# Kernel tuning notes

Measured on AMD Instinct MI355X. Metric: run time of the kernel, lower is better.

Reference implementation:

```python
import jax, jax.numpy as jnp
import numpy as np

N_NODES = 100000
N_EDGES = 1600000
D_IN = 64
D_HID = 64
D_OUT = 64
DROP_P = 0.5


def _degree_norms(src, dst, n):
    ones = jnp.ones(src.shape[0], dtype=jnp.float32)
    deg_out = jax.ops.segment_sum(ones, src, num_segments=n)  # out-degree of src nodes
    deg_in = jax.ops.segment_sum(ones, dst, num_segments=n)   # in-degree of dst nodes
    norm_src = jnp.where(deg_out > 0, jax.lax.rsqrt(jnp.maximum(deg_out, 1.0)), 0.0)
    norm_dst = jnp.where(deg_in > 0, jax.lax.rsqrt(jnp.maximum(deg_in, 1.0)), 0.0)
    return norm_src, norm_dst


def _graph_conv(h, W, b, src, dst, norm_src, norm_dst, n, activation=None):
    # DGL GraphConv, norm='both': out = D_in^{-1/2} A (D_out^{-1/2} h) W + b
    h = h * norm_src[:, None]
    h = h @ W                      # small GEMM first (in >= out), math-equivalent
    msg = h[src]                   # gather  [E, d]
    agg = jax.ops.segment_sum(msg, dst, num_segments=n)  # scatter-add [N, d]
    out = agg * norm_dst[:, None] + b
    if activation is not None:
        out = activation(out)
    return out


def _dropout(h, key, p=DROP_P):
    keep = jax.random.bernoulli(key, 1.0 - p, h.shape)
    return jnp.where(keep, h / (1.0 - p), 0.0)


def setup_inputs() -> dict:
    key = jax.random.key(0)
    ks = jax.random.split(key, 6)
    x = jax.random.normal(ks[0], (N_NODES, D_IN), dtype=jnp.float32)
    W0 = jax.random.normal(ks[1], (D_IN, D_HID), dtype=jnp.float32) * 0.05
    W1 = jax.random.normal(ks[2], (D_HID, D_HID), dtype=jnp.float32) * 0.05
    W2 = jax.random.normal(ks[3], (D_HID, D_OUT), dtype=jnp.float32) * 0.05
    b0 = jnp.zeros((D_HID,), dtype=jnp.float32)
    b1 = jnp.zeros((D_HID,), dtype=jnp.float32)
    b2 = jnp.zeros((D_OUT,), dtype=jnp.float32)
    src = jax.random.randint(ks[4], (N_EDGES,), 0, N_NODES, dtype=jnp.int32)
    dst = jax.random.randint(ks[5], (N_EDGES,), 0, N_NODES, dtype=jnp.int32)
    return {"x": x, "W0": W0, "b0": b0, "W1": W1, "b1": b1, "W2": W2, "b2": b2,
            "src": src, "dst": dst}


def reference(x, W0, b0, W1, b1, W2, b2, src, dst):
    n = x.shape[0]
    norm_src, norm_dst = _degree_norms(src, dst, n)
    dk = jax.random.key(1)
    h = _graph_conv(x, W0, b0, src, dst, norm_src, norm_dst, n, jax.nn.relu)
    h = _dropout(h, jax.random.fold_in(dk, 0))
    h = _graph_conv(h, W1, b1, src, dst, norm_src, norm_dst, n, jax.nn.relu)
    h = _dropout(h, jax.random.fold_in(dk, 1))
    h = _graph_conv(h, W2, b2, src, dst, norm_src, norm_dst, n, None)
    return h
```

## Files before the change

### kernel.cpp

```cpp
#include <hip/hip_runtime.h>
#include <hip/hip_bf16.h>
#include <hip/hip_fp16.h>
#include <cstddef>


#define WG 256
#define SLOT_S 48
#define NB_SHIFT 9
#define NB_W 512
#define EB 2048
#define PSTRIDE 257

__host__ __device__ static inline unsigned rotl32(unsigned x, int r) {
  return (x << r) | (x >> (32 - r));
}

__host__ __device__ static inline void threefry2x32(unsigned k0, unsigned k1,
                                                    unsigned x0, unsigned x1,
                                                    unsigned& o0, unsigned& o1) {
  unsigned ks2 = k0 ^ k1 ^ 0x1BD11BDAu;
  x0 += k0; x1 += k1;
#define TF_ROUND(r) { x0 += x1; x1 = rotl32(x1, r); x1 ^= x0; }
  TF_ROUND(13) TF_ROUND(15) TF_ROUND(26) TF_ROUND(6)
  x0 += k1;  x1 += ks2 + 1u;
  TF_ROUND(17) TF_ROUND(29) TF_ROUND(16) TF_ROUND(24)
  x0 += ks2; x1 += k0 + 2u;
  TF_ROUND(13) TF_ROUND(15) TF_ROUND(26) TF_ROUND(6)
  x0 += k0;  x1 += k1 + 3u;
  TF_ROUND(17) TF_ROUND(29) TF_ROUND(16) TF_ROUND(24)
  x0 += k1;  x1 += ks2 + 4u;
  TF_ROUND(13) TF_ROUND(15) TF_ROUND(26) TF_ROUND(6)
  x0 += ks2; x1 += k0 + 5u;
#undef TF_ROUND
  o0 = x0; o1 = x1;
}

__device__ static inline float2 h2f(unsigned u) {
  return __half22float2(__builtin_bit_cast(__half2, u));
}
__device__ static inline unsigned f2h(float a, float b) {
  return __builtin_bit_cast(unsigned, __floats2half2_rn(a, b));
}


__global__ __launch_bounds__(WG) void bin_k(
    const int* __restrict__ src, const int* __restrict__ dst,
    unsigned* __restrict__ binbuf_d, unsigned short* __restrict__ binbuf_s,
    unsigned short* __restrict__ pref_d, unsigned short* __restrict__ pref_s,
    int e) {
  __shared__ int hist_d[256], hist_s[256];
  __shared__ int scan_d[256], scan_s[256];
  __shared__ int curs_d[256], curs_s[256];
  __shared__ unsigned sorted_d[EB];
  __shared__ unsigned short sorted_s[EB];
  int tid = threadIdx.x;
  int blk = blockIdx.x;
  int base = blk * EB;
  int cnt = e - base;
  if (cnt > EB) cnt = EB;

  hist_d[tid] = 0;
  hist_s[tid] = 0;
  __syncthreads();
  for (int i = tid; i < cnt; i += WG) {
    int d = dst[base + i];
    int s = src[base + i];
    atomicAdd(&hist_d[d >> NB_SHIFT], 1);
    atomicAdd(&hist_s[s >> NB_SHIFT], 1);
  }
  __syncthreads();
  int hd = hist_d[tid], hs = hist_s[tid];
  scan_d[tid] = hd;
  scan_s[tid] = hs;
  __syncthreads();
  for (int st = 1; st < 256; st <<= 1) {
    int ad = (tid >= st) ? scan_d[tid - st] : 0;
    int as = (tid >= st) ? scan_s[tid - st] : 0;
    __syncthreads();
    scan_d[tid] += ad;
    scan_s[tid] += as;
    __syncthreads();
  }
  int ed = scan_d[tid] - hd;
  int es = scan_s[tid] - hs;
  curs_d[tid] = ed;
  curs_s[tid] = es;
  pref_d[(size_t)blk * PSTRIDE + tid] = (unsigned short)ed;
  pref_s[(size_t)blk * PSTRIDE + tid] = (unsigned short)es;
  if (tid == 255) {
    pref_d[(size_t)blk * PSTRIDE + 256] = (unsigned short)scan_d[255];
    pref_s[(size_t)blk * PSTRIDE + 256] = (unsigned short)scan_s[255];
  }
  __syncthreads();
  for (int i = tid; i < cnt; i += WG) {
    int d = dst[base + i];
    int s = src[base + i];
    int pd = atomicAdd(&curs_d[d >> NB_SHIFT], 1);
    sorted_d[pd] = ((unsigned)(d & (NB_W - 1)) << 17) | (unsigned)s;
    int ps = atomicAdd(&curs_s[s >> NB_SHIFT], 1);
    sorted_s[ps] = (unsigned short)(s & (NB_W - 1));
  }
  __syncthreads();
  for (int i = tid; i < cnt; i += WG) binbuf_d[base + i] = sorted_d[i];
  for (int i = tid; i < cnt; i += WG) binbuf_s[base + i] = sorted_s[i];
}


__global__ __launch_bounds__(WG) void debin_k(
    const unsigned* __restrict__ binbuf_d,
    const unsigned short* __restrict__ binbuf_s,
    const unsigned short* __restrict__ pref_d,
    const unsigned short* __restrict__ pref_s,
    int* __restrict__ slot, int* __restrict__ cnt_in,
    float* __restrict__ nsrc, const float* __restrict__ x,
    unsigned short* __restrict__ G0, int n, int nblk, int nbuck) {
  __shared__ int lcnt[NB_W];
  __shared__ float lns[NB_W];
  int tid = threadIdx.x;
  int b = blockIdx.x;
  for (int i = tid; i < NB_W; i += WG) lcnt[i] = 0;
  __syncthreads();
  if (b < nbuck) {
    for (int seg = tid; seg < nblk; seg += WG) {
      const unsigned short* pr = pref_d + (size_t)seg * PSTRIDE + b;
      int p0 = pr[0], p1 = pr[1];
      const unsigned* bb = binbuf_d + (size_t)seg * EB;
      for (int i = p0; i < p1; ++i) {
        unsigned v = bb[i];
        int dl = v >> 17;
        int s = (int)(v & 0x1FFFFu);
        int c = atomicAdd(&lcnt[dl], 1);
        if (c < SLOT_S) slot[(size_t)((b << NB_SHIFT) + dl) * SLOT_S + c] = s;
      }
    }
    __syncthreads();
    for (int i = tid; i < NB_W; i += WG) {
      int v = (b << NB_SHIFT) + i;
      if (v < n) cnt_in[v] = lcnt[i];
    }
  } else {
    int b2 = b - nbuck;
    for (int seg = tid; seg < nblk; seg += WG) {
      const unsigned short* pr = pref_s + (size_t)seg * PSTRIDE + b2;
      int p0 = pr[0], p1 = pr[1];
      const unsigned short* bb = binbuf_s + (size_t)seg * EB;
      for (int i = p0; i < p1; ++i) atomicAdd(&lcnt[bb[i]], 1);
    }
    __syncthreads();
    int vbase = b2 << NB_SHIFT;
    for (int i = tid; i < NB_W; i += WG) {
      int v = vbase + i;
      if (v < n) {
        int c = lcnt[i];
        float ns = (c > 0) ? rsqrtf((float)c) : 0.f;
        lns[i] = ns;
        nsrc[v] = ns;
      }
    }
    __syncthreads();
    const float4* x4 = (const float4*)x;
    uint2* G2 = (uint2*)G0;
    int lim = NB_W * 16;
    for (int idx = tid; idx < lim; idx += WG) {
      int nl = idx >> 4;
      int v = vbase + nl;
      if (v < n) {
        float ns = lns[nl];
        float4 r = x4[(size_t)v * 16 + (idx & 15)];
        G2[(size_t)v * 16 + (idx & 15)] =
            make_uint2(f2h(r.x * ns, r.y * ns), f2h(r.z * ns, r.w * ns));
      }
    }
  }
}

__global__ __launch_bounds__(WG) void layer_k(
    const unsigned short* __restrict__ G, const int* __restrict__ slot,
    const int* __restrict__ cnt_in, const float* __restrict__ nsrc,
    const float* __restrict__ W, const float* __restrict__ bias,
    unsigned short* __restrict__ GoutH, float* __restrict__ GoutF,
    int n, int mid, unsigned dk0, unsigned dk1) {
  __shared__ float4 Ws[1024];
  __shared__ __align__(16) float rows[4][272];
  const float4* W4 = (const float4*)W;
  for (int i = threadIdx.x; i < 1024; i += WG) Ws[i] = W4[i];

  int wave = threadIdx.x >> 6;
  int lane = threadIdx.x & 63;
  int g = lane >> 4;
  int l16 = lane & 15;
  int v = blockIdx.x * 16 + wave * 4 + g;
  bool valid = (v < n);
  int vc = valid ? v : (n - 1);

  int degt = valid ? cnt_in[vc] : 0;
  int deg = (degt > SLOT_S) ? SLOT_S : degt;
  const int* sl = slot + (size_t)vc * SLOT_S;
  const uint2* G2 = (const uint2*)G;

  float4 aA = make_float4(0.f, 0.f, 0.f, 0.f);
  float4 aB = make_float4(0.f, 0.f, 0.f, 0.f);
  float4 aC = make_float4(0.f, 0.f, 0.f, 0.f);
  float4 aD = make_float4(0.f, 0.f, 0.f, 0.f);
#define ACC(dst, m) { float2 lo = h2f((m).x), hi = h2f((m).y); \
    dst.x += lo.x; dst.y += lo.y; dst.z += hi.x; dst.w += hi.y; }
  int nq = deg >> 2;
  int i = 0;
  for (; i + 1 < nq; i += 2) {
    int4 q0 = *(const int4*)(sl + i * 4);
    int4 q1 = *(const int4*)(sl + i * 4 + 4);
    uint2 m0 = G2[(size_t)q0.x * 16 + l16];
    uint2 m1 = G2[(size_t)q0.y * 16 + l16];
    uint2 m2 = G2[(size_t)q0.z * 16 + l16];
    uint2 m3 = G2[(size_t)q0.w * 16 + l16];
    uint2 m4 = G2[(size_t)q1.x * 16 + l16];
    uint2 m5 = G2[(size_t)q1.y * 16 + l16];
    uint2 m6 = G2[(size_t)q1.z * 16 + l16];
    uint2 m7 = G2[(size_t)q1.w * 16 + l16];
    ACC(aA, m0) ACC(aB, m1) ACC(aC, m2) ACC(aD, m3)
    ACC(aA, m4) ACC(aB, m5) ACC(aC, m6) ACC(aD, m7)
  }
  if (i < nq) {
    int4 q0 = *(const int4*)(sl + i * 4);
    uint2 m0 = G2[(size_t)q0.x * 16 + l16];
    uint2 m1 = G2[(size_t)q0.y * 16 + l16];
    uint2 m2 = G2[(size_t)q0.z * 16 + l16];
    uint2 m3 = G2[(size_t)q0.w * 16 + l16];
    ACC(aA, m0) ACC(aB, m1) ACC(aC, m2) ACC(aD, m3)
  }
  int rem = deg & 3;
  if (rem) {
    int4 q = *(const int4*)(sl + (deg & ~3));
    int s0 = q.x;
    int s1 = (rem > 1) ? q.y : s0;
    int s2 = (rem > 2) ? q.z : s0;
    float w1 = (rem > 1) ? 1.f : 0.f;
    float w2 = (rem > 2) ? 1.f : 0.f;
    uint2 m0 = G2[(size_t)s0 * 16 + l16];
    uint2 m1 = G2[(size_t)s1 * 16 + l16];
    uint2 m2 = G2[(size_t)s2 * 16 + l16];
    ACC(aA, m0)
    { float2 lo = h2f(m1.x), hi = h2f(m1.y);
      aB.x = fmaf(w1, lo.x, aB.x); aB.y = fmaf(w1, lo.y, aB.y);
      aB.z = fmaf(w1, hi.x, aB.z); aB.w = fmaf(w1, hi.y, aB.w); }
    { float2 lo = h2f(m2.x), hi = h2f(m2.y);
      aC.x = fmaf(w2, lo.x, aC.x); aC.y = fmaf(w2, lo.y, aC.y);
      aC.z = fmaf(w2, hi.x, aC.z); aC.w = fmaf(w2, hi.y, aC.w); }
  }
#undef ACC
  float4 agg;
  agg.x = (aA.x + aB.x) + (aC.x + aD.x);
  agg.y = (aA.y + aB.y) + (aC.y + aD.y);
  agg.z = (aA.z + aB.z) + (aC.z + aD.z);
  agg.w = (aA.w + aB.w) + (aC.w + aD.w);

  float* rw = &rows[wave][g * 68];
  *(float4*)(rw + l16 * 4) = agg;
  __syncthreads();

  float4 acc = make_float4(0.f, 0.f, 0.f, 0.f);
#pragma unroll
  for (int k = 0; k < 64; ++k) {
    float a = rw[k];
    float4 w = Ws[k * 16 + l16];
    acc.x = fmaf(a, w.x, acc.x);
    acc.y = fmaf(a, w.y, acc.y);
    acc.z = fmaf(a, w.z, acc.z);
    acc.w = fmaf(a, w.w, acc.w);
  }

  float nd = (degt > 0) ? rsqrtf((float)degt) : 0.f;
  float4 b4 = ((const float4*)bias)[l16];
  float4 o;
  o.x = fmaf(acc.x, nd, b4.x);
  o.y = fmaf(acc.y, nd, b4.y);
  o.z = fmaf(acc.z, nd, b4.z);
  o.w = fmaf(acc.w, nd, b4.w);
  if (mid) {
    o.x = fmaxf(o.x, 0.f); o.y = fmaxf(o.y, 0.f);
    o.z = fmaxf(o.z, 0.f); o.w = fmaxf(o.w, 0.f);
    unsigned idx = (unsigned)(v * 64 + l16 * 4);
    unsigned r0a, r0b, r1a, r1b, r2a, r2b, r3a, r3b;
    threefry2x32(dk0, dk1, 0u, idx + 0u, r0a, r0b);
    threefry2x32(dk0, dk1, 0u, idx + 1u, r1a, r1b);
    threefry2x32(dk0, dk1, 0u, idx + 2u, r2a, r2b);
    threefry2x32(dk0, dk1, 0u, idx + 3u, r3a, r3b);
    float ns2 = 2.f * nsrc[vc];
    o.x = ((r0a ^ r0b) & 0x80000000u) ? 0.f : o.x * ns2;
    o.y = ((r1a ^ r1b) & 0x80000000u) ? 0.f : o.y * ns2;
    o.z = ((r2a ^ r2b) & 0x80000000u) ? 0.f : o.z * ns2;
    o.w = ((r3a ^ r3b) & 0x80000000u) ? 0.f : o.w * ns2;
    if (valid)
      ((uint2*)GoutH)[(size_t)v * 16 + l16] =
          make_uint2(f2h(o.x, o.y), f2h(o.z, o.w));
  } else {
    if (valid) ((float4*)GoutF)[(size_t)v * 16 + l16] = o;
  }
}


extern "C" void kernel_launch(void* const* d_in, const int* in_sizes, int n_in,
                              void* d_out, int out_size, void* d_ws, size_t ws_size,
                              hipStream_t stream) {
  const float* x  = (const float*)d_in[0];
  const float* W0 = (const float*)d_in[1];
  const float* b0 = (const float*)d_in[2];
  const float* W1 = (const float*)d_in[3];
  const float* b1 = (const float*)d_in[4];
  const float* W2 = (const float*)d_in[5];
  const float* b2 = (const float*)d_in[6];
  const int* src  = (const int*)d_in[7];
  const int* dst  = (const int*)d_in[8];
  float* out = (float*)d_out;

  const int n = in_sizes[0] / 64;
  const int e = in_sizes[7];
  const int nbuck = (n + NB_W - 1) / NB_W;
  const int nblk = (e + EB - 1) / EB;

  char* w = (char*)d_ws;
  size_t off = 0;
  auto alloc = [&](size_t bytes) -> void* {
    void* p = w + off;
    off += (bytes + 255) & ~(size_t)255;
    return p;
  };
  int*            cnt_in   = (int*)alloc((size_t)n * 4);
  float*          nsrc     = (float*)alloc((size_t)n * 4);
  unsigned*       binbuf_d = (unsigned*)alloc((size_t)nblk * EB * 4);
  unsigned short* binbuf_s = (unsigned short*)alloc((size_t)nblk * EB * 2);
  unsigned short* pref_d   = (unsigned short*)alloc((size_t)nblk * PSTRIDE * 2);
  unsigned short* pref_s   = (unsigned short*)alloc((size_t)nblk * PSTRIDE * 2);
  int*            slot     = (int*)alloc((size_t)nbuck * NB_W * SLOT_S * 4);
  unsigned short* G0       = (unsigned short*)alloc((size_t)n * 64 * 2);
  unsigned short* G1       = (unsigned short*)alloc((size_t)n * 64 * 2);

  unsigned k0a, k0b, k1a, k1b;
  threefry2x32(0u, 1u, 0u, 0u, k0a, k0b);
  threefry2x32(0u, 1u, 0u, 1u, k1a, k1b);

  const int gL = (n + 15) / 16;

  bin_k<<<nblk, WG, 0, stream>>>(src, dst, binbuf_d, binbuf_s,
                                 pref_d, pref_s, e);
  debin_k<<<2 * nbuck, WG, 0, stream>>>(binbuf_d, binbuf_s, pref_d, pref_s,
                                        slot, cnt_in, nsrc, x, G0,
                                        n, nblk, nbuck);

  layer_k<<<gL, WG, 0, stream>>>(G0, slot, cnt_in, nsrc, W0, b0, G1, nullptr,
                                 n, 1, k0a, k0b);
  layer_k<<<gL, WG, 0, stream>>>(G1, slot, cnt_in, nsrc, W1, b1, G0, nullptr,
                                 n, 1, k1a, k1b);
  layer_k<<<gL, WG, 0, stream>>>(G0, slot, cnt_in, nsrc, W2, b2, nullptr, out,
                                 n, 0, 0u, 0u);
}
```

Before: 290.7 us.

## Bin edges into per-bucket global regions via atomic cursors instead of prefix tables

Each bin block now reserves space in a per-bucket global buffer with an atomic add on padded bucket counters, then scatters its locally sorted edges there, using a binary search over the local scan to find each element's bucket. The debin pass then reads one contiguous region per bucket with all threads. Previously a single thread looped over each of roughly 800 segments serially. This removes the serial per-segment walk and the prefix tables, at the cost of global atomics, two memsets, and a fixed per-bucket capacity that silently drops edges if a bucket overflows.

```diff
diff --git a/kernel.cpp b/kernel.cpp
--- a/kernel.cpp
+++ b/kernel.cpp
@@ -9,7 +9,8 @@
 #define NB_SHIFT 9
 #define NB_W 512
 #define EB 2048
-#define PSTRIDE 257
+#define CAP 10240
+#define CPAD 16
 
 __host__ __device__ static inline unsigned rotl32(unsigned x, int r) {
   return (x << r) | (x >> (32 - r));
@@ -45,17 +46,17 @@
 
 __global__ __launch_bounds__(WG) void bin_k(
     const int* __restrict__ src, const int* __restrict__ dst,
+    int* __restrict__ bcnt_d, int* __restrict__ bcnt_s,
     unsigned* __restrict__ binbuf_d, unsigned short* __restrict__ binbuf_s,
-    unsigned short* __restrict__ pref_d, unsigned short* __restrict__ pref_s,
     int e) {
   __shared__ int hist_d[256], hist_s[256];
   __shared__ int scan_d[256], scan_s[256];
   __shared__ int curs_d[256], curs_s[256];
+  __shared__ int gb_d[256], gb_s[256];
   __shared__ unsigned sorted_d[EB];
   __shared__ unsigned short sorted_s[EB];
   int tid = threadIdx.x;
-  int blk = blockIdx.x;
-  int base = blk * EB;
+  int base = blockIdx.x * EB;
   int cnt = e - base;
   if (cnt > EB) cnt = EB;
 
@@ -81,16 +82,10 @@
     scan_s[tid] += as;
     __syncthreads();
   }
-  int ed = scan_d[tid] - hd;
-  int es = scan_s[tid] - hs;
-  curs_d[tid] = ed;
-  curs_s[tid] = es;
-  pref_d[(size_t)blk * PSTRIDE + tid] = (unsigned short)ed;
-  pref_s[(size_t)blk * PSTRIDE + tid] = (unsigned short)es;
-  if (tid == 255) {
-    pref_d[(size_t)blk * PSTRIDE + 256] = (unsigned short)scan_d[255];
-    pref_s[(size_t)blk * PSTRIDE + 256] = (unsigned short)scan_s[255];
-  }
+  curs_d[tid] = scan_d[tid] - hd;
+  curs_s[tid] = scan_s[tid] - hs;
+  if (hd > 0) gb_d[tid] = atomicAdd(&bcnt_d[tid * CPAD], hd);
+  if (hs > 0) gb_s[tid] = atomicAdd(&bcnt_s[tid * CPAD], hs);
   __syncthreads();
   for (int i = tid; i < cnt; i += WG) {
     int d = dst[base + i];
@@ -101,19 +96,36 @@
     sorted_s[ps] = (unsigned short)(s & (NB_W - 1));
   }
   __syncthreads();
-  for (int i = tid; i < cnt; i += WG) binbuf_d[base + i] = sorted_d[i];
-  for (int i = tid; i < cnt; i += WG) binbuf_s[base + i] = sorted_s[i];
+  for (int i = tid; i < cnt; i += WG) {
+    int lo = 0, hi = 255;
+    while (lo < hi) {
+      int mid = (lo + hi) >> 1;
+      if (scan_d[mid] > i) hi = mid; else lo = mid + 1;
+    }
+    int b = lo;
+    int pos = gb_d[b] + (i - (scan_d[b] - hist_d[b]));
+    if (pos < CAP) binbuf_d[(size_t)b * CAP + pos] = sorted_d[i];
+  }
+  for (int i = tid; i < cnt; i += WG) {
+    int lo = 0, hi = 255;
+    while (lo < hi) {
+      int mid = (lo + hi) >> 1;
+      if (scan_s[mid] > i) hi = mid; else lo = mid + 1;
+    }
+    int b = lo;
+    int pos = gb_s[b] + (i - (scan_s[b] - hist_s[b]));
+    if (pos < CAP) binbuf_s[(size_t)b * CAP + pos] = sorted_s[i];
+  }
 }
 
 
 __global__ __launch_bounds__(WG) void debin_k(
     const unsigned* __restrict__ binbuf_d,
     const unsigned short* __restrict__ binbuf_s,
-    const unsigned short* __restrict__ pref_d,
-    const unsigned short* __restrict__ pref_s,
+    const int* __restrict__ bcnt_d, const int* __restrict__ bcnt_s,
     int* __restrict__ slot, int* __restrict__ cnt_in,
     float* __restrict__ nsrc, const float* __restrict__ x,
-    unsigned short* __restrict__ G0, int n, int nblk, int nbuck) {
+    unsigned short* __restrict__ G0, int n, int nbuck) {
   __shared__ int lcnt[NB_W];
   __shared__ float lns[NB_W];
   int tid = threadIdx.x;
@@ -121,17 +133,15 @@
   for (int i = tid; i < NB_W; i += WG) lcnt[i] = 0;
   __syncthreads();
   if (b < nbuck) {
-    for (int seg = tid; seg < nblk; seg += WG) {
-      const unsigned short* pr = pref_d + (size_t)seg * PSTRIDE + b;
-      int p0 = pr[0], p1 = pr[1];
-      const unsigned* bb = binbuf_d + (size_t)seg * EB;
-      for (int i = p0; i < p1; ++i) {
-        unsigned v = bb[i];
-        int dl = v >> 17;
-        int s = (int)(v & 0x1FFFFu);
-        int c = atomicAdd(&lcnt[dl], 1);
-        if (c < SLOT_S) slot[(size_t)((b << NB_SHIFT) + dl) * SLOT_S + c] = s;
-      }
+    int m = bcnt_d[b * CPAD];
+    if (m > CAP) m = CAP;
+    const unsigned* bb = binbuf_d + (size_t)b * CAP;
+    for (int i = tid; i < m; i += WG) {
+      unsigned v = bb[i];
+      int dl = v >> 17;
+      int s = (int)(v & 0x1FFFFu);
+      int c = atomicAdd(&lcnt[dl], 1);
+      if (c < SLOT_S) slot[(size_t)((b << NB_SHIFT) + dl) * SLOT_S + c] = s;
     }
     __syncthreads();
     for (int i = tid; i < NB_W; i += WG) {
@@ -140,12 +150,10 @@
     }
   } else {
     int b2 = b - nbuck;
-    for (int seg = tid; seg < nblk; seg += WG) {
-      const unsigned short* pr = pref_s + (size_t)seg * PSTRIDE + b2;
-      int p0 = pr[0], p1 = pr[1];
-      const unsigned short* bb = binbuf_s + (size_t)seg * EB;
-      for (int i = p0; i < p1; ++i) atomicAdd(&lcnt[bb[i]], 1);
-    }
+    int m = bcnt_s[b2 * CPAD];
+    if (m > CAP) m = CAP;
+    const unsigned short* bb = binbuf_s + (size_t)b2 * CAP;
+    for (int i = tid; i < m; i += WG) atomicAdd(&lcnt[bb[i]], 1);
     __syncthreads();
     int vbase = b2 << NB_SHIFT;
     for (int i = tid; i < NB_W; i += WG) {
@@ -327,10 +335,10 @@
   };
   int*            cnt_in   = (int*)alloc((size_t)n * 4);
   float*          nsrc     = (float*)alloc((size_t)n * 4);
-  unsigned*       binbuf_d = (unsigned*)alloc((size_t)nblk * EB * 4);
-  unsigned short* binbuf_s = (unsigned short*)alloc((size_t)nblk * EB * 2);
-  unsigned short* pref_d   = (unsigned short*)alloc((size_t)nblk * PSTRIDE * 2);
-  unsigned short* pref_s   = (unsigned short*)alloc((size_t)nblk * PSTRIDE * 2);
+  int*            bcnt_d   = (int*)alloc(256 * CPAD * 4);
+  int*            bcnt_s   = (int*)alloc(256 * CPAD * 4);
+  unsigned*       binbuf_d = (unsigned*)alloc((size_t)nbuck * CAP * 4);
+  unsigned short* binbuf_s = (unsigned short*)alloc((size_t)nbuck * CAP * 2);
   int*            slot     = (int*)alloc((size_t)nbuck * NB_W * SLOT_S * 4);
   unsigned short* G0       = (unsigned short*)alloc((size_t)n * 64 * 2);
   unsigned short* G1       = (unsigned short*)alloc((size_t)n * 64 * 2);
@@ -341,11 +349,13 @@
 
   const int gL = (n + 15) / 16;
 
-  bin_k<<<nblk, WG, 0, stream>>>(src, dst, binbuf_d, binbuf_s,
-                                 pref_d, pref_s, e);
-  debin_k<<<2 * nbuck, WG, 0, stream>>>(binbuf_d, binbuf_s, pref_d, pref_s,
-                                        slot, cnt_in, nsrc, x, G0,
-                                        n, nblk, nbuck);
+  hipMemsetAsync(bcnt_d, 0, 256 * CPAD * 4, stream);
+  hipMemsetAsync(bcnt_s, 0, 256 * CPAD * 4, stream);
+
+  bin_k<<<nblk, WG, 0, stream>>>(src, dst, bcnt_d, bcnt_s,
+                                 binbuf_d, binbuf_s, e);
+  debin_k<<<2 * nbuck, WG, 0, stream>>>(binbuf_d, binbuf_s, bcnt_d, bcnt_s,
+                                        slot, cnt_in, nsrc, x, G0, n, nbuck);
 
   layer_k<<<gL, WG, 0, stream>>>(G0, slot, cnt_in, nsrc, W0, b0, G1, nullptr,
                                  n, 1, k0a, k0b);
```

Result: slower. 314.2 us (+8.1%).
